# Kernel optimization log

Measured on AMD Instinct MI355X. Metric: run time of the kernel, lower is better.

Reference implementation:

```python
import jax, jax.numpy as jnp
import numpy as np

BN_EPS = 1e-5


def _fps(xyz, n_centers):
    """Furthest point sampling. xyz: (B,N,3) -> idx (B,n_centers) int32.
    Deterministic start at index 0 (torch version uses randint start)."""
    B, N, _ = xyz.shape
    batch_ar = jnp.arange(B)

    def step(carry, _):
        distances, farthest = carry  # (B,N), (B,)
        center = xyz[batch_ar, farthest]  # (B,3)
        d = jnp.sum((xyz - center[:, None, :]) ** 2, axis=-1)  # (B,N)
        distances = jnp.minimum(distances, d)
        new_far = jnp.argmax(distances, axis=-1)
        return (distances, new_far), farthest

    init = (jnp.full((B, N), jnp.inf, dtype=xyz.dtype),
            jnp.zeros((B,), dtype=jnp.int32))
    _, idxs = jax.lax.scan(step, init, None, length=n_centers)  # (n_centers, B)
    return idxs.T  # (B, n_centers)


def _knn_group(xyz, centers, k):
    """xyz:(B,N,3), centers:(B,M,3) -> patches (B,M,k,3) center-relative."""
    # (B,M,N) squared distances
    dists = jnp.sum((centers[:, :, None, :] - xyz[:, None, :, :]) ** 2, axis=-1)
    _, idx = jax.lax.top_k(-dists, k)  # (B,M,k) smallest distances
    # gather neighbor coords: (B,M,k,3)
    patches = jnp.take_along_axis(xyz[:, None, :, :], idx[..., None], axis=2)
    return patches - centers[:, :, None, :]


def _bn_eval(x, gamma, beta):
    # BatchNorm1d in eval mode: running_mean=0, running_var=1
    return x * (gamma / jnp.sqrt(1.0 + BN_EPS)) + beta


def _mini_pointnet(patches, W1, b1, g1, bt1, W2, b2, g2, bt2, W3, b3, g3, bt3):
    B, M, k, C = patches.shape
    x = patches.reshape(B * M * k, C)
    x = jax.nn.relu(_bn_eval(x @ W1 + b1, g1, bt1))
    x = jax.nn.relu(_bn_eval(x @ W2 + b2, g2, bt2))
    x = jax.nn.relu(_bn_eval(x @ W3 + b3, g3, bt3))
    x = x.reshape(B * M, k, -1).max(axis=1)
    return x.reshape(B, M, -1)


def setup_inputs() -> dict:
    key = jax.random.key(0)
    ks = jax.random.split(key, 8)
    B, N = 16, 16384
    embed = 256

    def lin(kk, fan_in, fan_out):
        bound = 1.0 / np.sqrt(fan_in)
        k1, k2 = jax.random.split(kk)
        W = jax.random.uniform(k1, (fan_in, fan_out), jnp.float32, -bound, bound)
        b = jax.random.uniform(k2, (fan_out,), jnp.float32, -bound, bound)
        return W, b

    W1, b1 = lin(ks[1], 3, 64)
    W2, b2 = lin(ks[2], 64, 128)
    W3, b3 = lin(ks[3], 128, embed)
    return {
        "xyz": jax.random.normal(ks[0], (B, N, 3), jnp.float32),
        "W1": W1, "b1": b1, "g1": jnp.ones((64,)), "bt1": jnp.zeros((64,)),
        "W2": W2, "b2": b2, "g2": jnp.ones((128,)), "bt2": jnp.zeros((128,)),
        "W3": W3, "b3": b3, "g3": jnp.ones((embed,)), "bt3": jnp.zeros((embed,)),
        "n_centers": 256,
        "k": 32,
    }


def reference(xyz, W1, b1, g1, bt1, W2, b2, g2, bt2, W3, b3, g3, bt3,
              n_centers, k):
    center_idx = _fps(xyz, n_centers)  # (B, M)
    centers = jnp.take_along_axis(xyz, center_idx[..., None], axis=1)  # (B,M,3)
    patches = _knn_group(xyz, centers, k)  # (B,M,k,3)
    tokens = _mini_pointnet(patches, W1, b1, g1, bt1, W2, b2, g2, bt2,
                            W3, b3, g3, bt3)
    return tokens, centers
```

## Files before the change

kernel.cpp:

```cpp
#include <hip/hip_runtime.h>

constexpr int B   = 16;
constexpr int N   = 16384;
constexpr int M   = 256;
constexpr int K   = 32;
constexpr int EMB = 256;

__device__ __forceinline__ float sqdist(float px, float py, float pz,
                                        float cx, float cy, float cz) {
  float dx = __fsub_rn(px, cx);
  float dy = __fsub_rn(py, cy);
  float dz = __fsub_rn(pz, cz);
  return __fadd_rn(__fadd_rn(__fmul_rn(dx, dx), __fmul_rn(dy, dy)),
                   __fmul_rn(dz, dz));
}

constexpr int FT = 512;
constexpr int FP = N / FT;
constexpr int FW = FT / 64;
static_assert(FT == 512 && FP == 32, "macro expansion assumes 512x32");

#define FPS_REP(X) X(0) X(1) X(2) X(3) X(4) X(5) X(6) X(7) X(8) X(9) \
  X(10) X(11) X(12) X(13) X(14) X(15) X(16) X(17) X(18) X(19) \
  X(20) X(21) X(22) X(23) X(24) X(25) X(26) X(27) X(28) X(29) X(30) X(31)

__global__ __launch_bounds__(FT, 2) void fps_kernel(
    const float* __restrict__ xyz, float* __restrict__ centers) {
  const int b = blockIdx.x;
  const int tid = threadIdx.x;
  const float* base = xyz + (size_t)b * N * 3;

#define FPS_DECL(i) float px##i, py##i, pz##i, ds##i;
  FPS_REP(FPS_DECL)
#undef FPS_DECL

#define FPS_LOAD(i) { const int n = tid + (i) * FT;      \
    px##i = base[n * 3 + 0];                              \
    py##i = base[n * 3 + 1];                              \
    pz##i = base[n * 3 + 2];                              \
    ds##i = __builtin_inff(); }
  FPS_REP(FPS_LOAD)
#undef FPS_LOAD

  __shared__ float s_pv[2][FW];
  __shared__ int s_pn[2][FW];

  float cx = base[0], cy = base[1], cz = base[2];

  for (int it = 0; it < M; ++it) {
    if (tid == 0) {
      float* co = centers + ((size_t)b * M + it) * 3;
      co[0] = cx; co[1] = cy; co[2] = cz;
    }
    const int p = it & 1;

    float bv = -1.0f;
    int bj = 0;
#define FPS_UPD(i) {                                       \
    float dx = __fsub_rn(px##i, cx);                       \
    float dy = __fsub_rn(py##i, cy);                       \
    float dz = __fsub_rn(pz##i, cz);                       \
    float dd = __fadd_rn(__fadd_rn(__fmul_rn(dx, dx),      \
                                   __fmul_rn(dy, dy)),     \
                         __fmul_rn(dz, dz));               \
    float nd = fminf(ds##i, dd);                           \
    ds##i = nd;                                            \
    bool g = nd > bv;                                      \
    bv = g ? nd : bv;                                      \
    bj = g ? (i) : bj; }
    FPS_REP(FPS_UPD)
#undef FPS_UPD
    int bn = (bj << 9) + tid;

#pragma unroll
    for (int mm = 32; mm >= 1; mm >>= 1) {
      float ov = __shfl_xor(bv, mm, 64);
      int on = __shfl_xor(bn, mm, 64);
      if (ov > bv || (ov == bv && on < bn)) { bv = ov; bn = on; }
    }
    if ((tid & 63) == 0) {
      s_pv[p][tid >> 6] = bv;
      s_pn[p][tid >> 6] = bn;
    }
    __syncthreads();

    float v = s_pv[p][0];
    int n = s_pn[p][0];
#pragma unroll
    for (int w = 1; w < FW; ++w) {
      float ov = s_pv[p][w];
      int on = s_pn[p][w];
      if (ov > v || (ov == v && on < n)) { v = ov; n = on; }
    }
    cx = base[(size_t)n * 3 + 0];
    cy = base[(size_t)n * 3 + 1];
    cz = base[(size_t)n * 3 + 2];
  }
}

constexpr int KT = 256;
constexpr int CAP = 512;
constexpr int NBUCKET = 1024;

__global__ __launch_bounds__(KT) void knn_kernel(
    const float* __restrict__ xyz, const float* __restrict__ centers,
    float* __restrict__ patches) {
  const int blk = blockIdx.x;
  const int b = blk >> 8;
  const int tid = threadIdx.x;
  const float* base = xyz + (size_t)b * N * 3;

  __shared__ int hist[NBUCKET];
  __shared__ unsigned cb[CAP];
  __shared__ int ci[CAP];
  __shared__ int s_nin, s_ncand, s_tb;
  __shared__ int s_wsum[KT / 64];
  __shared__ float s_cc[3];

  if (tid == 0) {
    const float* c = centers + (size_t)blk * 3;
    s_cc[0] = c[0]; s_cc[1] = c[1]; s_cc[2] = c[2];
    s_nin = 0; s_ncand = 0;
  }
  for (int i = tid; i < NBUCKET; i += KT) hist[i] = 0;
  __syncthreads();

  const float cx = s_cc[0], cy = s_cc[1], cz = s_cc[2];

  for (int n = tid; n < N; n += KT) {
    float d = sqdist(base[n * 3], base[n * 3 + 1], base[n * 3 + 2], cx, cy, cz);
    atomicAdd(&hist[__float_as_uint(d) >> 21], 1);
  }
  __syncthreads();

  int h0[4];
  int loc = 0;
#pragma unroll
  for (int i = 0; i < 4; ++i) { h0[i] = hist[tid * 4 + i]; loc += h0[i]; }
  int lane = tid & 63, wid = tid >> 6;
  int scan = loc;
  for (int off = 1; off < 64; off <<= 1) {
    int o = __shfl_up(scan, off, 64);
    if (lane >= off) scan += o;
  }
  if (lane == 63) s_wsum[wid] = scan;
  __syncthreads();
  int woff = 0;
  for (int w = 0; w < wid; ++w) woff += s_wsum[w];
  int c0 = woff + scan - loc;
#pragma unroll
  for (int i = 0; i < 4; ++i) {
    int c1 = c0 + h0[i];
    if (c0 < K && c1 >= K) s_tb = tid * 4 + i;
    c0 = c1;
  }
  __syncthreads();
  const int tb = s_tb;
  const unsigned lo = (unsigned)tb << 21;
  const unsigned hi = (unsigned)(tb + 1) << 21;

  for (int n = tid; n < N; n += KT) {
    float x = base[n * 3], y = base[n * 3 + 1], z = base[n * 3 + 2];
    float d = sqdist(x, y, z, cx, cy, cz);
    unsigned bits = __float_as_uint(d);
    if (bits < lo) {
      int pos = atomicAdd(&s_nin, 1);
      float* p = patches + ((size_t)blk * K + pos) * 3;
      p[0] = __fsub_rn(x, cx); p[1] = __fsub_rn(y, cy); p[2] = __fsub_rn(z, cz);
    } else if (bits < hi) {
      int q = atomicAdd(&s_ncand, 1);
      if (q < CAP) { cb[q] = bits; ci[q] = n; }
    }
  }
  __syncthreads();

  const int nin = s_nin;
  const int ncand = min(s_ncand, CAP);
  const int nsel = K - nin;
  for (int j = tid; j < ncand; j += KT) {
    unsigned bj = cb[j];
    int ij = ci[j];
    int rank = 0;
    for (int i2 = 0; i2 < ncand; ++i2) {
      unsigned bv = cb[i2];
      int iv = ci[i2];
      rank += (bv < bj || (bv == bj && iv < ij)) ? 1 : 0;
    }
    if (rank < nsel) {
      float x = base[ij * 3], y = base[ij * 3 + 1], z = base[ij * 3 + 2];
      float* p = patches + ((size_t)blk * K + nin + rank) * 3;
      p[0] = __fsub_rn(x, cx); p[1] = __fsub_rn(y, cy); p[2] = __fsub_rn(z, cz);
    }
  }
}

constexpr int MT = 128;

__global__ __launch_bounds__(MT) void mlp_kernel(
    const float* __restrict__ patches,
    const float* __restrict__ W1, const float* __restrict__ b1,
    const float* __restrict__ g1, const float* __restrict__ bt1,
    const float* __restrict__ W2, const float* __restrict__ b2,
    const float* __restrict__ g2, const float* __restrict__ bt2,
    const float* __restrict__ W3, const float* __restrict__ b3,
    const float* __restrict__ g3, const float* __restrict__ bt3,
    float* __restrict__ tokens) {
  const int pm = blockIdx.x;
  const int tid = threadIdx.x;
  __shared__ float xs[3][K];
  __shared__ float h1s[64 * K];
  __shared__ float h2s[128 * K];
  __shared__ float pms[2][EMB];

  const float* patch = patches + (size_t)pm * (K * 3);
  if (tid < 96) xs[tid % 3][tid / 3] = patch[tid];
  __syncthreads();

  const int cg = tid & 63;
  const int half = tid >> 6;
  const int pt0 = half * 16;
  const float rs = 1.0f / sqrtf(1.0f + 1e-5f);

  {
    const int c = cg;
    const float w0 = W1[c], w1 = W1[64 + c], w2 = W1[128 + c];
    const float bb = b1[c];
    const float sc = g1[c] * rs, be = bt1[c];
    float o[16];
#pragma unroll
    for (int p = 0; p < 16; ++p) {
      int pt = pt0 + p;
      float a = xs[0][pt] * w0 + xs[1][pt] * w1 + xs[2][pt] * w2 + bb;
      o[p] = fmaxf(a * sc + be, 0.0f);
    }
    const int so = (c & 7) << 2;
#pragma unroll
    for (int p4 = 0; p4 < 16; p4 += 4) {
      *(float4*)&h1s[c * K + ((pt0 + p4) ^ so)] =
          make_float4(o[p4], o[p4 + 1], o[p4 + 2], o[p4 + 3]);
    }
  }
  __syncthreads();

  {
    const int c = cg * 2;
    float acc0[16], acc1[16];
    const float bb0 = b2[c], bb1 = b2[c + 1];
#pragma unroll
    for (int p = 0; p < 16; ++p) { acc0[p] = bb0; acc1[p] = bb1; }
    for (int k = 0; k < 64; ++k) {
      const float2 w = *(const float2*)(W2 + k * 128 + c);
      const int so = (k & 7) << 2;
      float4 x0 = *(const float4*)&h1s[k * K + ((pt0 + 0) ^ so)];
      float4 x1 = *(const float4*)&h1s[k * K + ((pt0 + 4) ^ so)];
      float4 x2 = *(const float4*)&h1s[k * K + ((pt0 + 8) ^ so)];
      float4 x3 = *(const float4*)&h1s[k * K + ((pt0 + 12) ^ so)];
      float xv[16] = {x0.x, x0.y, x0.z, x0.w, x1.x, x1.y, x1.z, x1.w,
                      x2.x, x2.y, x2.z, x2.w, x3.x, x3.y, x3.z, x3.w};
#pragma unroll
      for (int p = 0; p < 16; ++p) {
        acc0[p] += xv[p] * w.x;
        acc1[p] += xv[p] * w.y;
      }
    }
    const float sc0 = g2[c] * rs, be0 = bt2[c];
    const float sc1 = g2[c + 1] * rs, be1 = bt2[c + 1];
    float o0[16], o1[16];
#pragma unroll
    for (int p = 0; p < 16; ++p) {
      o0[p] = fmaxf(acc0[p] * sc0 + be0, 0.0f);
      o1[p] = fmaxf(acc1[p] * sc1 + be1, 0.0f);
    }
    const int soa = (c & 7) << 2, sob = ((c + 1) & 7) << 2;
#pragma unroll
    for (int p4 = 0; p4 < 16; p4 += 4) {
      *(float4*)&h2s[c * K + ((pt0 + p4) ^ soa)] =
          make_float4(o0[p4], o0[p4 + 1], o0[p4 + 2], o0[p4 + 3]);
      *(float4*)&h2s[(c + 1) * K + ((pt0 + p4) ^ sob)] =
          make_float4(o1[p4], o1[p4 + 1], o1[p4 + 2], o1[p4 + 3]);
    }
  }
  __syncthreads();

  {
    const int c = cg * 4;
    float acc[4][16];
#pragma unroll
    for (int i = 0; i < 4; ++i) {
      const float bb = b3[c + i];
#pragma unroll
      for (int p = 0; p < 16; ++p) acc[i][p] = bb;
    }
    for (int k = 0; k < 128; ++k) {
      const float4 w = *(const float4*)(W3 + (size_t)k * 256 + c);
      const int so = (k & 7) << 2;
      float4 x0 = *(const float4*)&h2s[k * K + ((pt0 + 0) ^ so)];
      float4 x1 = *(const float4*)&h2s[k * K + ((pt0 + 4) ^ so)];
      float4 x2 = *(const float4*)&h2s[k * K + ((pt0 + 8) ^ so)];
      float4 x3 = *(const float4*)&h2s[k * K + ((pt0 + 12) ^ so)];
      float xv[16] = {x0.x, x0.y, x0.z, x0.w, x1.x, x1.y, x1.z, x1.w,
                      x2.x, x2.y, x2.z, x2.w, x3.x, x3.y, x3.z, x3.w};
#pragma unroll
      for (int p = 0; p < 16; ++p) {
        acc[0][p] += xv[p] * w.x;
        acc[1][p] += xv[p] * w.y;
        acc[2][p] += xv[p] * w.z;
        acc[3][p] += xv[p] * w.w;
      }
    }
#pragma unroll
    for (int i = 0; i < 4; ++i) {
      const float sc = g3[c + i] * rs, be = bt3[c + i];
      float mx = 0.0f;
#pragma unroll
      for (int p = 0; p < 16; ++p)
        mx = fmaxf(mx, fmaxf(acc[i][p] * sc + be, 0.0f));
      pms[half][c + i] = mx;
    }
  }
  __syncthreads();

  {
    const int c2 = tid * 2;
    float* to = tokens + (size_t)pm * EMB;
    to[c2] = fmaxf(pms[0][c2], pms[1][c2]);
    to[c2 + 1] = fmaxf(pms[0][c2 + 1], pms[1][c2 + 1]);
  }
}

extern "C" void kernel_launch(void* const* d_in, const int* in_sizes, int n_in,
                              void* d_out, int out_size, void* d_ws,
                              size_t ws_size, hipStream_t stream) {
  const float* xyz = (const float*)d_in[0];
  const float* W1 = (const float*)d_in[1];
  const float* b1 = (const float*)d_in[2];
  const float* g1 = (const float*)d_in[3];
  const float* bt1 = (const float*)d_in[4];
  const float* W2 = (const float*)d_in[5];
  const float* b2 = (const float*)d_in[6];
  const float* g2 = (const float*)d_in[7];
  const float* bt2 = (const float*)d_in[8];
  const float* W3 = (const float*)d_in[9];
  const float* b3 = (const float*)d_in[10];
  const float* g3 = (const float*)d_in[11];
  const float* bt3 = (const float*)d_in[12];

  float* tokens = (float*)d_out;
  float* centers = tokens + (size_t)B * M * EMB;
  float* patches = (float*)d_ws;

  fps_kernel<<<B, FT, 0, stream>>>(xyz, centers);
  knn_kernel<<<B * M, KT, 0, stream>>>(xyz, centers, patches);
  mlp_kernel<<<B * M, MT, 0, stream>>>(patches, W1, b1, g1, bt1, W2, b2, g2,
                                       bt2, W3, b3, g3, bt3, tokens);
}
```

Measured before the change: 812.2 us.

## Restructure FPS to 1024 threads with contiguous float4 reloads per iteration

```diff
diff --git a/kernel.cpp b/kernel.cpp
--- a/kernel.cpp
+++ b/kernel.cpp
@@ -15,37 +15,29 @@
                    __fmul_rn(dz, dz));
 }
 
-constexpr int FT = 512;
-constexpr int FP = N / FT;
+constexpr int FT = 1024;
 constexpr int FW = FT / 64;
-static_assert(FT == 512 && FP == 32, "macro expansion assumes 512x32");
-
-#define FPS_REP(X) X(0) X(1) X(2) X(3) X(4) X(5) X(6) X(7) X(8) X(9) \
-  X(10) X(11) X(12) X(13) X(14) X(15) X(16) X(17) X(18) X(19) \
-  X(20) X(21) X(22) X(23) X(24) X(25) X(26) X(27) X(28) X(29) X(30) X(31)
-
-__global__ __launch_bounds__(FT, 2) void fps_kernel(
+
+#define FPS_REP16(X) X(0) X(1) X(2) X(3) X(4) X(5) X(6) X(7) X(8) X(9) \
+  X(10) X(11) X(12) X(13) X(14) X(15)
+
+__global__ __launch_bounds__(FT) void fps_kernel(
     const float* __restrict__ xyz, float* __restrict__ centers) {
   const int b = blockIdx.x;
   const int tid = threadIdx.x;
   const float* base = xyz + (size_t)b * N * 3;
-
-#define FPS_DECL(i) float px##i, py##i, pz##i, ds##i;
-  FPS_REP(FPS_DECL)
+  const float4* b4 = (const float4*)base;
+
+#define FPS_DECL(i) float ds##i = __builtin_inff();
+  FPS_REP16(FPS_DECL)
 #undef FPS_DECL
-
-#define FPS_LOAD(i) { const int n = tid + (i) * FT;      \
-    px##i = base[n * 3 + 0];                              \
-    py##i = base[n * 3 + 1];                              \
-    pz##i = base[n * 3 + 2];                              \
-    ds##i = __builtin_inff(); }
-  FPS_REP(FPS_LOAD)
-#undef FPS_LOAD
 
   __shared__ float s_pv[2][FW];
   __shared__ int s_pn[2][FW];
 
   float cx = base[0], cy = base[1], cz = base[2];
+
+  const int f0 = tid * 12;
 
   for (int it = 0; it < M; ++it) {
     if (tid == 0) {
@@ -56,21 +48,37 @@
 
     float bv = -1.0f;
     int bj = 0;
-#define FPS_UPD(i) {                                       \
-    float dx = __fsub_rn(px##i, cx);                       \
-    float dy = __fsub_rn(py##i, cy);                       \
-    float dz = __fsub_rn(pz##i, cz);                       \
+
+#define FPS_UPD(dn, j, X, Y, Z) {                          \
+    float dx = __fsub_rn((X), cx);                         \
+    float dy = __fsub_rn((Y), cy);                         \
+    float dz = __fsub_rn((Z), cz);                         \
     float dd = __fadd_rn(__fadd_rn(__fmul_rn(dx, dx),      \
                                    __fmul_rn(dy, dy)),     \
                          __fmul_rn(dz, dz));               \
-    float nd = fminf(ds##i, dd);                           \
-    ds##i = nd;                                            \
+    float nd = fminf(dn, dd);                              \
+    dn = nd;                                               \
     bool g = nd > bv;                                      \
     bv = g ? nd : bv;                                      \
-    bj = g ? (i) : bj; }
-    FPS_REP(FPS_UPD)
+    bj = g ? (j) : bj; }
+
+#define FPS_CHUNK(c, dA, dB, dC, dD) {                     \
+    float4 qa = b4[f0 + (c) * 3 + 0];                      \
+    float4 qb = b4[f0 + (c) * 3 + 1];                      \
+    float4 qc = b4[f0 + (c) * 3 + 2];                      \
+    FPS_UPD(dA, (c) * 4 + 0, qa.x, qa.y, qa.z)             \
+    FPS_UPD(dB, (c) * 4 + 1, qa.w, qb.x, qb.y)             \
+    FPS_UPD(dC, (c) * 4 + 2, qb.z, qb.w, qc.x)             \
+    FPS_UPD(dD, (c) * 4 + 3, qc.y, qc.z, qc.w) }
+
+    FPS_CHUNK(0, ds0, ds1, ds2, ds3)
+    FPS_CHUNK(1, ds4, ds5, ds6, ds7)
+    FPS_CHUNK(2, ds8, ds9, ds10, ds11)
+    FPS_CHUNK(3, ds12, ds13, ds14, ds15)
+#undef FPS_CHUNK
 #undef FPS_UPD
-    int bn = (bj << 9) + tid;
+
+    int bn = (tid << 4) + bj;
 
 #pragma unroll
     for (int mm = 32; mm >= 1; mm >>= 1) {
@@ -78,10 +86,7 @@
       int on = __shfl_xor(bn, mm, 64);
       if (ov > bv || (ov == bv && on < bn)) { bv = ov; bn = on; }
     }
-    if ((tid & 63) == 0) {
-      s_pv[p][tid >> 6] = bv;
-      s_pn[p][tid >> 6] = bn;
-    }
+    if ((tid & 63) == 0) { s_pv[p][tid >> 6] = bv; s_pn[p][tid >> 6] = bn; }
     __syncthreads();
 
     float v = s_pv[p][0];
```

After: 947.3 us. 1.17x slower.
